# Kernel optimization log

Hardware: AMD Instinct MI355X
Metric: run time of the kernel (lower is better)

## Reference

```python
import jax, jax.numpy as jnp
import numpy as np

B, N, C, H = 8, 1024, 768, 12
WBITS, ABITS, PGABITS = 8, 8, 4
TH = 0.99  # greater-than mask threshold on MSB softmax


def quant(x, bits):
    """Fixed-point quantize to `bits` bits, straight-through estimator."""
    step = 2.0 ** (1 - bits)
    q = jnp.round(x / step) * step
    return x + jax.lax.stop_gradient(q - x)


def setup_inputs() -> dict:
    key = jax.random.key(0)
    k1, k2, k3 = jax.random.split(key, 3)
    x = jax.random.normal(k1, (B, N, C), jnp.float32)
    # qkv: QLinear(dim, 3*dim, bias=False); proj: QLinear(dim, dim, bias=True)
    w_qkv = jax.random.normal(k2, (3 * C, C), jnp.float32) * (C ** -0.5)
    w_proj = jax.random.normal(k3, (C, C), jnp.float32) * (C ** -0.5)
    b_proj = jnp.zeros((C,), jnp.float32)
    return {"x": x, "w_qkv": w_qkv, "w_proj": w_proj, "b_proj": b_proj}


def reference(x, w_qkv, w_proj, b_proj):
    d = C // H
    scale = d ** -0.5
    # QLinear: quantize activations and weights, then matmul (no qkv bias)
    qkv = quant(x, ABITS) @ quant(w_qkv, WBITS).T            # [B,N,3C]
    qkv = qkv.reshape(B, N, 3, H, d).transpose(2, 0, 3, 1, 4)  # [3,B,H,N,d]
    qkv = quant(qkv, ABITS)
    q, k, v = qkv[0], qkv[1], qkv[2]
    # low-precision MSB pass
    q_msb = quant(q, PGABITS)
    k_msb = quant(k, PGABITS)
    attn_msb = jax.nn.softmax(
        jnp.einsum('bhqd,bhkd->bhqk', q_msb, k_msb) * scale, axis=-1)
    # GreaterThan with straight-through backward (identity grad)
    gt = (attn_msb > TH).astype(attn_msb.dtype)
    mask = attn_msb + jax.lax.stop_gradient(gt - attn_msb)
    # full-precision pass, masked pre-softmax
    attn = jnp.einsum('bhqd,bhkd->bhqk', q, k) * scale * mask
    attn = quant(jax.nn.softmax(attn, axis=-1), ABITS)
    out = jnp.einsum('bhqk,bhkd->bhqd', attn, v)             # [B,H,N,d]
    out = out.transpose(0, 2, 1, 3).reshape(B, N, C)
    return quant(out, ABITS) @ quant(w_proj, WBITS).T + b_proj
```

## Files before the change

### kernel.cpp

```cpp
#include <hip/hip_runtime.h>

#define NB 8
#define NSEQ 1024
#define NC 768
#define NH 12
#define ND 64
#define NM 8192

typedef _Float16 v8h __attribute__((ext_vector_type(8)));
typedef float v4f __attribute__((ext_vector_type(4)));
typedef int   v4i __attribute__((ext_vector_type(4)));

__device__ __forceinline__ float q8f(float x){ return rintf(x*128.f)*0.0078125f; }
__device__ __forceinline__ int imax2(int a, int b){ return a > b ? a : b; }
__device__ __forceinline__ int imin2(int a, int b){ return a < b ? a : b; }

__device__ __forceinline__ int swz(int r, int g){ return (r<<6) + (((g ^ (r & 7)) & 7)<<3); }

__device__ __forceinline__ int idot64(const int* a, const int* b) {
  int si = 0;
#if __has_builtin(__builtin_amdgcn_sdot4)
#pragma unroll
  for (int j = 0; j < 16; j++) si = __builtin_amdgcn_sdot4(a[j], b[j], si, false);
#else
  const char* ca = (const char*)a;
  const char* cb = (const char*)b;
#pragma unroll
  for (int j = 0; j < 64; j++) si += (int)ca[j] * (int)cb[j];
#endif
  return si;
}

__device__ __forceinline__ void async_cp16(const void* g, void* l) {
  __builtin_amdgcn_global_load_lds(
      (const __attribute__((address_space(1))) unsigned int*)g,
      (__attribute__((address_space(3))) unsigned int*)l, 16, 0, 0);
}

__global__ __launch_bounds__(512, 2) void k_qk(const float* __restrict__ x,
                                               const float* __restrict__ wqkv,
                                               const float* __restrict__ bias,
                                               char* __restrict__ QmI,
                                               char* __restrict__ KmI,
                                               float* __restrict__ out) {
  if (blockIdx.x >= 192) {
    int gid = (blockIdx.x - 192)*512 + threadIdx.x;
    int c4 = gid % 192;
    ((float4*)out)[gid] = ((const float4*)bias)[c4];
    return;
  }
  __shared__ _Float16 S[65536];
  _Float16* SA = S;
  _Float16* SB = S + 32768;

  const int tid  = threadIdx.x;
  const int lane = tid & 63;
  const int quad = lane >> 4;
  const int l15  = lane & 15;
  const int wid  = tid >> 6;
  const int wm   = wid >> 2;
  const int wn   = wid & 3;
  const int bx = blockIdx.x & 31, by = blockIdx.x >> 5;
  const int m0 = bx * 256, n0 = by * 256;

  const int h   = tid >> 8;
  const int t2  = tid & 255;
  const int rr_ = t2 >> 1;
  const int gp  = (t2 & 1) * 4;

  auto ldq = [&](const float* src, int row0, int kc, int g0, float4* f) {
    const float* sp = src + (size_t)(row0 + h*128 + rr_)*768 + kc*64 + g0*8;
    f[0] = ((const float4*)sp)[0]; f[1] = ((const float4*)sp)[1];
    f[2] = ((const float4*)sp)[2]; f[3] = ((const float4*)sp)[3];
  };
  auto wrq = [&](_Float16* dstbuf, int g0, const float4* f) {
#pragma unroll
    for (int gi = 0; gi < 2; gi++) {
      const float* ff = (const float*)&f[gi*2];
      v8h o;
#pragma unroll
      for (int j = 0; j < 8; j++) o[j] = (_Float16)q8f(ff[j]);
      *(v8h*)&dstbuf[h*8192 + swz(rr_, g0 + gi)] = o;
    }
  };

  v4f acc[8][4] = {};
  float4 fa[4], fb[4];

  ldq(x,    m0, 0, gp,     fa);  wrq(SA, gp,     fa);
  ldq(x,    m0, 0, gp + 2, fa);  wrq(SA, gp + 2, fa);
  ldq(wqkv, n0, 0, gp,     fb);  wrq(SB, gp,     fb);
  ldq(wqkv, n0, 0, gp + 2, fb);  wrq(SB, gp + 2, fb);
  __syncthreads();

#pragma unroll 1
  for (int kc = 0; kc < 12; kc++) {
    const int buf = kc & 1;
    const _Float16* A  = &SA[(buf*2 + wm)*8192];
    const _Float16* Bh = &SB[(buf*2 + (wn>>1))*8192];
    _Float16* SAn = &SA[(buf^1)*16384];
    _Float16* SBn = &SB[(buf^1)*16384];
    const bool pre = (kc + 1 < 12);

    if (pre) ldq(x, m0, kc + 1, gp, fa);

    v8h bf[4][2];
#pragma unroll
    for (int nt = 0; nt < 4; nt++)
#pragma unroll
      for (int ks = 0; ks < 2; ks++)
        bf[nt][ks] = *(const v8h*)&Bh[swz((wn&1)*64 + nt*16 + l15, ks*4 + quad)];

#pragma unroll
    for (int p = 0; p < 4; p++) {
      v8h a[2][2];
#pragma unroll
      for (int mt = 0; mt < 2; mt++)
#pragma unroll
        for (int ks = 0; ks < 2; ks++)
          a[mt][ks] = *(const v8h*)&A[swz((p*2 + mt)*16 + l15, ks*4 + quad)];
      __builtin_amdgcn_s_setprio(1);
#pragma unroll
      for (int ks = 0; ks < 2; ks++)
#pragma unroll
        for (int nt = 0; nt < 4; nt++) {
          acc[p*2+0][nt] = __builtin_amdgcn_mfma_f32_16x16x32_f16(a[0][ks], bf[nt][ks], acc[p*2+0][nt], 0, 0, 0);
          acc[p*2+1][nt] = __builtin_amdgcn_mfma_f32_16x16x32_f16(a[1][ks], bf[nt][ks], acc[p*2+1][nt], 0, 0, 0);
        }
      __builtin_amdgcn_s_setprio(0);
      if (pre) {
        if (p == 0) { wrq(SAn, gp,     fa); ldq(x,    m0, kc + 1, gp + 2, fa); }
        if (p == 1) { wrq(SAn, gp + 2, fa); ldq(wqkv, n0, kc + 1, gp,     fb); }
        if (p == 2) { wrq(SBn, gp,     fb); ldq(wqkv, n0, kc + 1, gp + 2, fb); }
        if (p == 3) { wrq(SBn, gp + 2, fb); }
      }
    }
    __syncthreads();
  }

  char* P8 = (char*)S;
#pragma unroll
  for (int fr = 0; fr < 8; fr++)
#pragma unroll
    for (int nt = 0; nt < 4; nt++)
#pragma unroll
      for (int rr = 0; rr < 4; rr++) {
        float v = q8f(acc[fr][nt][rr]);
        int qi = (int)rintf(v * 8.f);
        int rl = wm*128 + fr*16 + quad*4 + rr;
        int cl = wn*64 + nt*16 + l15;
        P8[rl*272 + cl] = (char)qi;
      }
  __syncthreads();
  const int which = (by >= 3);
  int c0 = n0 - which*768;
#pragma unroll
  for (int t = 0; t < 8; t++) {
    int idx = tid + t*512;
    int r = idx >> 4, cg = idx & 15;
    v4i val = *(const v4i*)&P8[r*272 + cg*16];
    if (!which) {
      *(v4i*)&QmI[(size_t)(m0 + r)*768 + c0 + cg*16] = val;
    } else {
      int m = m0 + r, n = m & 1023, bI = m >> 10;
      int col = c0 + cg*16;
      int hh = col >> 6, d0 = col & 63;
      *(v4i*)&KmI[(((size_t)(bI*NH + hh)*1024 + n) << 6) + d0] = val;
    }
  }
}

__global__ __launch_bounds__(256) void k_attn(const char* __restrict__ QmI,
                                              const char* __restrict__ KmI,
                                              const float* __restrict__ x,
                                              const float* __restrict__ wqkv,
                                              const float* __restrict__ wproj,
                                              float* __restrict__ out) {
  __shared__ char  S2[2][16384];
  __shared__ float rowm[128];
  __shared__ int   cand[128];
  __shared__ int   hrowA[128];
  __shared__ int   hcolA[128];
  __shared__ float qf[64], kf[64], vf[64];
  __shared__ float od[64];
  __shared__ float pps;
  __shared__ int   cnt, hcnt;

  const int tid  = threadIdx.x;
  const int lane = tid & 63;
  const int quad = lane >> 4;
  const int l15  = lane & 15;
  const int wid  = tid >> 6;
  const int R0   = wid * 16;
  const int bh = blockIdx.x;
  const int q0 = blockIdx.y * 128;
  const int bb = bh / NH, hb = bh % NH;
  const size_t mrow = (size_t)bb * NSEQ;
  const int hoff = hb * 64;
  const char* KmB = KmI + (size_t)bh * 1024 * 64;

  if (tid == 0) { cnt = 0; hcnt = 0; }

  auto stageK = [&](int kp, int bi) {
#pragma unroll
    for (int s = 0; s < 4; s++) {
      int seg = wid*4 + s;
      async_cp16(KmB + kp*16384 + seg*1024 + lane*16, &S2[bi][seg*1024]);
    }
  };

  v4i aQ[2];
#pragma unroll
  for (int b2 = 0; b2 < 2; b2++)
    aQ[b2] = *(const v4i*)&QmI[(mrow + q0 + b2*64 + R0 + l15)*768 + hoff + quad*16];

  int lm[2][4], lm2[2][4];
#pragma unroll
  for (int b2 = 0; b2 < 2; b2++)
#pragma unroll
    for (int r = 0; r < 4; r++) { lm[b2][r] = -1073741824; lm2[b2][r] = -1073741824; }

  stageK(0, 0);
#pragma unroll 1
  for (int kp = 0; kp < 4; kp++) {
    if (kp + 1 < 4) {
      stageK(kp + 1, (kp + 1) & 1);
      asm volatile("s_waitcnt vmcnt(4)" ::: "memory");
    } else {
      asm volatile("s_waitcnt vmcnt(0)" ::: "memory");
    }
    __builtin_amdgcn_s_barrier();
#pragma unroll
    for (int g64 = 0; g64 < 4; g64++) {
      const char* Ks = &S2[kp & 1][g64*4096];
      v4i c0a[4] = {}, c1a[4] = {};
      __builtin_amdgcn_s_setprio(1);
#pragma unroll
      for (int nt = 0; nt < 4; nt++) {
        v4i b = *(const v4i*)&Ks[(nt*16 + l15)*64 + quad*16];
        c0a[nt] = __builtin_amdgcn_mfma_i32_16x16x64_i8(aQ[0], b, c0a[nt], 0, 0, 0);
        c1a[nt] = __builtin_amdgcn_mfma_i32_16x16x64_i8(aQ[1], b, c1a[nt], 0, 0, 0);
      }
      __builtin_amdgcn_s_setprio(0);
#pragma unroll
      for (int r = 0; r < 4; r++) {
        int g0 = imax2(imax2(c0a[0][r], c0a[1][r]), imax2(c0a[2][r], c0a[3][r]));
        lm2[0][r] = imax2(lm2[0][r], imin2(lm[0][r], g0));
        lm[0][r]  = imax2(lm[0][r], g0);
        int g1 = imax2(imax2(c1a[0][r], c1a[1][r]), imax2(c1a[2][r], c1a[3][r]));
        lm2[1][r] = imax2(lm2[1][r], imin2(lm[1][r], g1));
        lm[1][r]  = imax2(lm[1][r], g1);
      }
    }
    __builtin_amdgcn_s_barrier();
  }
#pragma unroll
  for (int b2 = 0; b2 < 2; b2++)
#pragma unroll
    for (int r = 0; r < 4; r++) {
      int m = lm[b2][r], m2 = lm2[b2][r];
#pragma unroll
      for (int o = 1; o < 16; o <<= 1) {
        int om  = __shfl_xor(m, o);
        int om2 = __shfl_xor(m2, o);
        m2 = imax2(imax2(m2, om2), imin2(m, om));
        m  = imax2(m, om);
      }
      if (l15 == 0 && (m - m2) > 2304) {
        int row = b2*64 + R0 + quad*4 + r;
        rowm[row] = (float)m * 0.001953125f;
        int ix = atomicAdd(&cnt, 1);
        cand[ix] = row;
      }
    }
  __syncthreads();

  int nc = cnt;
  for (int ci = wid; ci < nc; ci += 4) {
    int row = cand[ci];
    float m = rowm[row];
    const int* qrow = (const int*)&QmI[(mrow + q0 + row)*768 + hoff];
    int qw[16];
#pragma unroll
    for (int j = 0; j < 16; j++) qw[j] = qrow[j];
    float l = 0.f, bmax = -1e30f;
    int bcol = 0;
    for (int t = 0; t < 16; t++) {
      const int* kb = (const int*)&KmB[(size_t)(t*64 + lane)*64];
      int si = idot64(qw, kb);
      float s = (float)si * 0.001953125f;
      l += expf(s - m);
      if (s > bmax) { bmax = s; bcol = t*64 + lane; }
    }
#pragma unroll
    for (int o = 1; o < 64; o <<= 1) {
      l += __shfl_xor(l, o);
      float ov = __shfl_xor(bmax, o);
      int   oc = __shfl_xor(bcol, o);
      if (ov > bmax || (ov == bmax && oc < bcol)) { bmax = ov; bcol = oc; }
    }
    if (lane == 0 && (1.0f / l) > 0.99f) {
      int ix = atomicAdd(&hcnt, 1);
      hrowA[ix] = row; hcolA[ix] = bcol;
    }
  }
  __syncthreads();

  int nh = hcnt;
  for (int hi = 0; hi < nh; hi++) {
    int row = hrowA[hi], cst = hcolA[hi];
    if (tid < 192) {
      int d = tid & 63, part = tid >> 6;
      int wrow = part*768 + hoff + d;
      int xrow = (part == 0) ? (int)(mrow + q0 + row) : (int)(mrow + cst);
      const float* xr2 = &x[(size_t)xrow*768];
      const float* wr = &wqkv[(size_t)wrow*768];
      float s = 0.f;
      for (int k = 0; k < 768; k++) s += q8f(xr2[k]) * q8f(wr[k]);
      float v = q8f(s);
      if (part == 0) qf[d] = v; else if (part == 1) kf[d] = v; else vf[d] = v;
    }
    __syncthreads();
    if (tid == 0) {
      float s = 0.f;
      for (int d = 0; d < 64; d++) s += qf[d]*kf[d];
      float sf = s * 0.125f;
      float m2 = fmaxf(sf, 0.f);
      float l2 = expf(sf - m2) + 1023.f*expf(-m2);
      pps = rintf(expf(sf - m2)/l2*128.f)*0.0078125f;
    }
    __syncthreads();
    float p = pps;
    if (p != 0.f) {
      if (tid < 64) od[tid] = q8f(p * vf[tid]);
      __syncthreads();
      for (int c = tid; c < 768; c += 256) {
        const float* wr = &wproj[(size_t)c*768 + hoff];
        float s = 0.f;
        for (int d = 0; d < 64; d++) s += od[d] * q8f(wr[d]);
        atomicAdd(&out[(mrow + q0 + row)*768 + c], s);
      }
    }
    __syncthreads();
  }
}

extern "C" void kernel_launch(void* const* d_in, const int* in_sizes, int n_in,
                              void* d_out, int out_size, void* d_ws, size_t ws_size,
                              hipStream_t stream) {
  const float* x      = (const float*)d_in[0];
  const float* w_qkv  = (const float*)d_in[1];
  const float* w_proj = (const float*)d_in[2];
  const float* b_proj = (const float*)d_in[3];
  float* out = (float*)d_out;

  char* p = (char*)d_ws;
  char* QmI = p;  p += (size_t)NM*768;
  char* KmI = p;  p += (size_t)NM*768;

  k_qk  <<<dim3(192 + 3072), dim3(512), 0, stream>>>(x, w_qkv, b_proj, QmI, KmI, out);
  k_attn<<<dim3(96, 8), dim3(256), 0, stream>>>(QmI, KmI, x, w_qkv, w_proj, out);
}
```

Before: 148.9 us.

## Prefetch whole K-chunk in fewer wider loads and drop min-occupancy launch bound

The QKV GEMM prefetch now loads each thread's full 32-float slice per operand in one batch of eight float4 loads, instead of four interleaved half-loads spread across the MFMA sub-steps. The B operand is written to LDS after the MFMA loop. This cuts the number of load/convert/store phases and gives the compiler more freedom over registers, helped by dropping the min-2-blocks launch bound. In exchange, global-load latency is hidden behind less MFMA work, and register pressure and occupancy may change.

```diff
diff --git a/kernel.cpp b/kernel.cpp
--- a/kernel.cpp
+++ b/kernel.cpp
@@ -37,12 +37,12 @@
       (__attribute__((address_space(3))) unsigned int*)l, 16, 0, 0);
 }
 
-__global__ __launch_bounds__(512, 2) void k_qk(const float* __restrict__ x,
-                                               const float* __restrict__ wqkv,
-                                               const float* __restrict__ bias,
-                                               char* __restrict__ QmI,
-                                               char* __restrict__ KmI,
-                                               float* __restrict__ out) {
+__global__ __launch_bounds__(512) void k_qk(const float* __restrict__ x,
+                                            const float* __restrict__ wqkv,
+                                            const float* __restrict__ bias,
+                                            char* __restrict__ QmI,
+                                            char* __restrict__ KmI,
+                                            float* __restrict__ out) {
   if (blockIdx.x >= 192) {
     int gid = (blockIdx.x - 192)*512 + threadIdx.x;
     int c4 = gid % 192;
@@ -68,29 +68,27 @@
   const int rr_ = t2 >> 1;
   const int gp  = (t2 & 1) * 4;
 
-  auto ldq = [&](const float* src, int row0, int kc, int g0, float4* f) {
-    const float* sp = src + (size_t)(row0 + h*128 + rr_)*768 + kc*64 + g0*8;
-    f[0] = ((const float4*)sp)[0]; f[1] = ((const float4*)sp)[1];
-    f[2] = ((const float4*)sp)[2]; f[3] = ((const float4*)sp)[3];
+  auto ldq8 = [&](const float* src, int row0, int kc, float4* f) {
+    const float* sp = src + (size_t)(row0 + h*128 + rr_)*768 + kc*64 + gp*8;
+#pragma unroll
+    for (int i = 0; i < 8; i++) f[i] = ((const float4*)sp)[i];
   };
-  auto wrq = [&](_Float16* dstbuf, int g0, const float4* f) {
-#pragma unroll
-    for (int gi = 0; gi < 2; gi++) {
+  auto wrq4 = [&](_Float16* dstbuf, const float4* f) {
+#pragma unroll
+    for (int gi = 0; gi < 4; gi++) {
       const float* ff = (const float*)&f[gi*2];
       v8h o;
 #pragma unroll
       for (int j = 0; j < 8; j++) o[j] = (_Float16)q8f(ff[j]);
-      *(v8h*)&dstbuf[h*8192 + swz(rr_, g0 + gi)] = o;
+      *(v8h*)&dstbuf[h*8192 + swz(rr_, gp + gi)] = o;
     }
   };
 
   v4f acc[8][4] = {};
-  float4 fa[4], fb[4];
-
-  ldq(x,    m0, 0, gp,     fa);  wrq(SA, gp,     fa);
-  ldq(x,    m0, 0, gp + 2, fa);  wrq(SA, gp + 2, fa);
-  ldq(wqkv, n0, 0, gp,     fb);  wrq(SB, gp,     fb);
-  ldq(wqkv, n0, 0, gp + 2, fb);  wrq(SB, gp + 2, fb);
+  float4 fs[8];
+
+  ldq8(x,    m0, 0, fs);  wrq4(SA, fs);
+  ldq8(wqkv, n0, 0, fs);  wrq4(SB, fs);
   __syncthreads();
 
 #pragma unroll 1
@@ -102,7 +100,7 @@
     _Float16* SBn = &SB[(buf^1)*16384];
     const bool pre = (kc + 1 < 12);
 
-    if (pre) ldq(x, m0, kc + 1, gp, fa);
+    if (pre) ldq8(x, m0, kc + 1, fs);
 
     v8h bf[4][2];
 #pragma unroll
@@ -128,13 +126,12 @@
           acc[p*2+1][nt] = __builtin_amdgcn_mfma_f32_16x16x32_f16(a[1][ks], bf[nt][ks], acc[p*2+1][nt], 0, 0, 0);
         }
       __builtin_amdgcn_s_setprio(0);
-      if (pre) {
-        if (p == 0) { wrq(SAn, gp,     fa); ldq(x,    m0, kc + 1, gp + 2, fa); }
-        if (p == 1) { wrq(SAn, gp + 2, fa); ldq(wqkv, n0, kc + 1, gp,     fb); }
-        if (p == 2) { wrq(SBn, gp,     fb); ldq(wqkv, n0, kc + 1, gp + 2, fb); }
-        if (p == 3) { wrq(SBn, gp + 2, fb); }
-      }
-    }
+      if (p == 0 && pre) {
+        wrq4(SAn, fs);
+        ldq8(wqkv, n0, kc + 1, fs);
+      }
+    }
+    if (pre) wrq4(SBn, fs);
     __syncthreads();
   }
 
```

New measurement: 153.1 us. 1.03x slower.
